# Kernel optimization log

Hardware: AMD Instinct MI355X
Metric: run time of the kernel (lower is better)

Reference implementation:

```python
import jax, jax.numpy as jnp
import numpy as np

D, P, R, K = 1024, 256, 64, 1024  # directions, sampling points, rank, subcarriers

def setup_inputs() -> dict:
    key = jax.random.key(0)
    k1, k2, k3 = jax.random.split(key, 3)
    return {
        "attenuation_vectors": jax.random.normal(k1, (D, P, R), dtype=jnp.float32),
        "radiation_vectors": jax.random.normal(k2, (D, P, R), dtype=jnp.float32),
        "frequency_basis_vectors": jax.random.normal(k3, (K, R), dtype=jnp.float32),
    }

def reference(attenuation_vectors, radiation_vectors, frequency_basis_vectors):
    # Original (per ray d, per subcarrier k):
    #   atten_factor[d,k] = sum_p sum_r u_rho[d,p,r] * F[k,r]
    #   rad_factor[d,k]   = sum_p sum_r u_s[d,p,r]   * F[k,r]
    #   csi[k] = (1/D) * sum_d atten_factor[d,k] * rad_factor[d,k]
    # Vectorized as two contractions over (p, r) plus a reduction over d.
    A = jnp.einsum('dpr,kr->dk', attenuation_vectors, frequency_basis_vectors)
    B = jnp.einsum('dpr,kr->dk', radiation_vectors, frequency_basis_vectors)
    num_directions = attenuation_vectors.shape[0]
    csi = jnp.sum(A * B, axis=0) / num_directions  # [K]
    return csi
```

## Files before the change

kernel.cpp:

```cpp
#include <hip/hip_runtime.h>

#define D_DIRS 1024
#define P_PTS  256
#define R_RANK 64
#define K_SUB  1024

typedef float v4f __attribute__((ext_vector_type(4)));

#define WS_A 0
#define WS_B (D_DIRS * R_RANK)
#define WS_M (2 * D_DIRS * R_RANK)
#define WS_MSUM 0
#define NB_B 32
#define DCHUNK (D_DIRS / NB_B)

__device__ __forceinline__ v4f ntload(const v4f* __restrict__ p) {
    return __builtin_nontemporal_load(p);
}

__device__ __forceinline__ v4f shfl_xor_v4(v4f v, int m) {
    v4f r;
    r.x = __shfl_xor(v.x, m);
    r.y = __shfl_xor(v.y, m);
    r.z = __shfl_xor(v.z, m);
    r.w = __shfl_xor(v.w, m);
    return r;
}

__global__ __launch_bounds__(512) void k_reduce_p(const float* __restrict__ atten,
                                                  const float* __restrict__ rad,
                                                  float* __restrict__ ws) {
    const int bid  = blockIdx.x;
    const int t    = threadIdx.x;
    const int lane = t & 63;
    const int wave = t >> 6;
    const int rq   = t & 15;

    const v4f* A4 = (const v4f*)atten;
    const v4f* B4 = (const v4f*)rad;

    __shared__ v4f lA[2][8][16];
    __shared__ v4f lB[2][8][16];

    const int d0 = bid * 4;

    v4f a_cur[8], b_cur[8], a_nxt[8], b_nxt[8];
    {
        const v4f* pa = A4 + (size_t)d0 * 4096 + t;
        const v4f* pb = B4 + (size_t)d0 * 4096 + t;
#pragma unroll
        for (int k = 0; k < 8; ++k) a_cur[k] = ntload(pa + k * 512);
#pragma unroll
        for (int k = 0; k < 8; ++k) b_cur[k] = ntload(pb + k * 512);
    }

#pragma unroll
    for (int dd = 0; dd < 4; ++dd) {
        const int d = d0 + dd;

        if (dd < 3) {
            const v4f* na = A4 + (size_t)(d + 1) * 4096 + t;
            const v4f* nb = B4 + (size_t)(d + 1) * 4096 + t;
#pragma unroll
            for (int k = 0; k < 8; ++k) a_nxt[k] = ntload(na + k * 512);
#pragma unroll
            for (int k = 0; k < 8; ++k) b_nxt[k] = ntload(nb + k * 512);
        }

        v4f sa = ((a_cur[0] + a_cur[1]) + (a_cur[2] + a_cur[3])) +
                 ((a_cur[4] + a_cur[5]) + (a_cur[6] + a_cur[7]));
        v4f sb = ((b_cur[0] + b_cur[1]) + (b_cur[2] + b_cur[3])) +
                 ((b_cur[4] + b_cur[5]) + (b_cur[6] + b_cur[7]));

        sa = sa + shfl_xor_v4(sa, 16);
        sa = sa + shfl_xor_v4(sa, 32);
        sb = sb + shfl_xor_v4(sb, 16);
        sb = sb + shfl_xor_v4(sb, 32);

        if ((lane >> 4) == 0) {
            lA[dd & 1][wave][rq] = sa;
            lB[dd & 1][wave][rq] = sb;
        }
        __syncthreads();

        if (t < 16) {
            v4f s = lA[dd & 1][0][t];
#pragma unroll
            for (int w = 1; w < 8; ++w) s = s + lA[dd & 1][w][t];
            ((v4f*)(ws + WS_A))[d * 16 + t] = s;
        } else if (t >= 64 && t < 80) {
            const int q = t - 64;
            v4f s = lB[dd & 1][0][q];
#pragma unroll
            for (int w = 1; w < 8; ++w) s = s + lB[dd & 1][w][q];
            ((v4f*)(ws + WS_B))[d * 16 + q] = s;
        }

#pragma unroll
        for (int k = 0; k < 8; ++k) { a_cur[k] = a_nxt[k]; b_cur[k] = b_nxt[k]; }
    }
}

__global__ __launch_bounds__(256) void k_partial_m(float* __restrict__ ws) {
    const int bb = blockIdx.x;
    const int t  = threadIdx.x;

    __shared__ float sa[DCHUNK * R_RANK];
    __shared__ float sb[DCHUNK * R_RANK];

    const float4* a4 = (const float4*)(ws + WS_A) + bb * (DCHUNK * R_RANK / 4);
    const float4* b4 = (const float4*)(ws + WS_B) + bb * (DCHUNK * R_RANK / 4);
    float4* sa4 = (float4*)sa;
    float4* sb4 = (float4*)sb;
    sa4[t]       = a4[t];
    sa4[t + 256] = a4[t + 256];
    sb4[t]       = b4[t];
    sb4[t + 256] = b4[t + 256];
    __syncthreads();

    const int c  = t & 63;
    const int wg = t >> 6;

    float acc[16];
#pragma unroll
    for (int i = 0; i < 16; ++i) acc[i] = 0.f;

    for (int dd = 0; dd < DCHUNK; ++dd) {
        const float bv = sb[dd * 64 + c];
        const float4* ar = (const float4*)&sa[dd * 64 + wg * 16];
        const float4 a0 = ar[0], a1 = ar[1], a2 = ar[2], a3 = ar[3];
        acc[0]  += a0.x * bv; acc[1]  += a0.y * bv; acc[2]  += a0.z * bv; acc[3]  += a0.w * bv;
        acc[4]  += a1.x * bv; acc[5]  += a1.y * bv; acc[6]  += a1.z * bv; acc[7]  += a1.w * bv;
        acc[8]  += a2.x * bv; acc[9]  += a2.y * bv; acc[10] += a2.z * bv; acc[11] += a2.w * bv;
        acc[12] += a3.x * bv; acc[13] += a3.y * bv; acc[14] += a3.z * bv; acc[15] += a3.w * bv;
    }

    float* Mp = ws + WS_M + bb * 4096;
#pragma unroll
    for (int i = 0; i < 16; ++i) Mp[(wg * 16 + i) * 64 + c] = acc[i];
}

__global__ __launch_bounds__(256) void k_reduce_m(float* __restrict__ ws) {
    const int tg = blockIdx.x * 256 + threadIdx.x;
    const float4* Mp4 = (const float4*)(ws + WS_M);
    float4 s = make_float4(0.f, 0.f, 0.f, 0.f);
#pragma unroll
    for (int g = 0; g < NB_B; ++g) {
        const float4 v = Mp4[g * 1024 + tg];
        s.x += v.x; s.y += v.y; s.z += v.z; s.w += v.w;
    }
    ((float4*)(ws + WS_MSUM))[tg] = s;
}

__global__ __launch_bounds__(256) void k_csi(const float* __restrict__ ws,
                                             const float* __restrict__ freq,
                                             float* __restrict__ out) {
    const int bb = blockIdx.x;
    const int t  = threadIdx.x;

    __shared__ float Ms[64 * 68];
    __shared__ float Fs[64 * 65];
    __shared__ float red[4][64];

    const float4* M4 = (const float4*)(ws + WS_MSUM);
#pragma unroll
    for (int i = 0; i < 4; ++i) {
        const int idx4 = i * 256 + t;
        const float4 s = M4[idx4];
        const int r = idx4 >> 4, c4 = idx4 & 15;
        *(float4*)&Ms[r * 68 + c4 * 4] = s;
    }

    const float4* F4 = (const float4*)freq + bb * 1024;
#pragma unroll
    for (int i = 0; i < 4; ++i) {
        const int idx4 = i * 256 + t;
        const float4 v = F4[idx4];
        const int row = idx4 >> 4, c4 = idx4 & 15;
        Fs[row * 65 + c4 * 4 + 0] = v.x;
        Fs[row * 65 + c4 * 4 + 1] = v.y;
        Fs[row * 65 + c4 * 4 + 2] = v.z;
        Fs[row * 65 + c4 * 4 + 3] = v.w;
    }
    __syncthreads();

    const int kl = t & 63;
    const int jg = t >> 6;

    float h[16];
#pragma unroll
    for (int j = 0; j < 16; ++j) h[j] = 0.f;

    for (int r = 0; r < 64; ++r) {
        const float fv = Fs[kl * 65 + r];
        const float4* mr = (const float4*)&Ms[r * 68 + jg * 16];
        const float4 m0 = mr[0], m1 = mr[1], m2 = mr[2], m3 = mr[3];
        h[0]  += fv * m0.x; h[1]  += fv * m0.y; h[2]  += fv * m0.z; h[3]  += fv * m0.w;
        h[4]  += fv * m1.x; h[5]  += fv * m1.y; h[6]  += fv * m1.z; h[7]  += fv * m1.w;
        h[8]  += fv * m2.x; h[9]  += fv * m2.y; h[10] += fv * m2.z; h[11] += fv * m2.w;
        h[12] += fv * m3.x; h[13] += fv * m3.y; h[14] += fv * m3.z; h[15] += fv * m3.w;
    }

    float part = 0.f;
#pragma unroll
    for (int j = 0; j < 16; ++j) part += h[j] * Fs[kl * 65 + jg * 16 + j];

    red[jg][kl] = part;
    __syncthreads();
    if (t < 64) {
        out[bb * 64 + t] =
            (red[0][t] + red[1][t] + red[2][t] + red[3][t]) * (1.0f / (float)D_DIRS);
    }
}

extern "C" void kernel_launch(void* const* d_in, const int* in_sizes, int n_in,
                              void* d_out, int out_size, void* d_ws, size_t ws_size,
                              hipStream_t stream) {
    const float* atten = (const float*)d_in[0];
    const float* rad   = (const float*)d_in[1];
    const float* freq  = (const float*)d_in[2];
    float* out = (float*)d_out;
    float* ws  = (float*)d_ws;

    k_reduce_p<<<D_DIRS / 4, 512, 0, stream>>>(atten, rad, ws);
    k_partial_m<<<NB_B, 256, 0, stream>>>(ws);
    k_reduce_m<<<4, 256, 0, stream>>>(ws);
    k_csi<<<16, 256, 0, stream>>>(ws, freq, out);
}
```

Before: 153.7 us.

## Remap P-reduction so each wave pair owns one direction, removing LDS and barriers

The sum over sampling points is reorganized so that each direction is handled by two waves, each owning half of the rank columns. Every lane accumulates 32 points across four prefetched chunks and finishes with in-wave xor shuffles, so the shared-memory staging and per-direction __syncthreads are gone. Each lane now reads 128-byte segments instead of fully contiguous 512-thread rows, which may change coalescing. The kernel is memory bound at 512MB, so the gain depends mostly on how well memory stays saturated.

```diff
diff --git a/kernel.cpp b/kernel.cpp
--- a/kernel.cpp
+++ b/kernel.cpp
@@ -30,74 +30,54 @@
 __global__ __launch_bounds__(512) void k_reduce_p(const float* __restrict__ atten,
                                                   const float* __restrict__ rad,
                                                   float* __restrict__ ws) {
-    const int bid  = blockIdx.x;
     const int t    = threadIdx.x;
+    const int wave = t >> 6;
     const int lane = t & 63;
-    const int wave = t >> 6;
-    const int rq   = t & 15;
-
-    const v4f* A4 = (const v4f*)atten;
-    const v4f* B4 = (const v4f*)rad;
-
-    __shared__ v4f lA[2][8][16];
-    __shared__ v4f lB[2][8][16];
-
-    const int d0 = bid * 4;
-
-    v4f a_cur[8], b_cur[8], a_nxt[8], b_nxt[8];
-    {
-        const v4f* pa = A4 + (size_t)d0 * 4096 + t;
-        const v4f* pb = B4 + (size_t)d0 * 4096 + t;
-#pragma unroll
-        for (int k = 0; k < 8; ++k) a_cur[k] = ntload(pa + k * 512);
-#pragma unroll
-        for (int k = 0; k < 8; ++k) b_cur[k] = ntload(pb + k * 512);
-    }
-
-#pragma unroll
-    for (int dd = 0; dd < 4; ++dd) {
-        const int d = d0 + dd;
-
-        if (dd < 3) {
-            const v4f* na = A4 + (size_t)(d + 1) * 4096 + t;
-            const v4f* nb = B4 + (size_t)(d + 1) * 4096 + t;
-#pragma unroll
-            for (int k = 0; k < 8; ++k) a_nxt[k] = ntload(na + k * 512);
-#pragma unroll
-            for (int k = 0; k < 8; ++k) b_nxt[k] = ntload(nb + k * 512);
+    const int d    = blockIdx.x * 4 + (wave >> 1);
+    const int half = wave & 1;
+    const int r4g  = lane & 7;
+    const int pr   = lane >> 3;
+
+    const int base = pr * 16 + half * 8 + r4g;
+    const v4f* A4 = (const v4f*)atten + (size_t)d * 4096 + base;
+    const v4f* B4 = (const v4f*)rad   + (size_t)d * 4096 + base;
+
+    v4f pa[8], pb[8], na[8], nb[8];
+#pragma unroll
+    for (int j = 0; j < 8; ++j) pa[j] = ntload(A4 + j * 128);
+#pragma unroll
+    for (int j = 0; j < 8; ++j) pb[j] = ntload(B4 + j * 128);
+
+    v4f acc_a = {0.f, 0.f, 0.f, 0.f};
+    v4f acc_b = {0.f, 0.f, 0.f, 0.f};
+
+#pragma unroll
+    for (int mc = 0; mc < 4; ++mc) {
+        if (mc < 3) {
+            const int off = (mc + 1) * 8 * 128;
+#pragma unroll
+            for (int j = 0; j < 8; ++j) na[j] = ntload(A4 + off + j * 128);
+#pragma unroll
+            for (int j = 0; j < 8; ++j) nb[j] = ntload(B4 + off + j * 128);
         }
-
-        v4f sa = ((a_cur[0] + a_cur[1]) + (a_cur[2] + a_cur[3])) +
-                 ((a_cur[4] + a_cur[5]) + (a_cur[6] + a_cur[7]));
-        v4f sb = ((b_cur[0] + b_cur[1]) + (b_cur[2] + b_cur[3])) +
-                 ((b_cur[4] + b_cur[5]) + (b_cur[6] + b_cur[7]));
-
-        sa = sa + shfl_xor_v4(sa, 16);
-        sa = sa + shfl_xor_v4(sa, 32);
-        sb = sb + shfl_xor_v4(sb, 16);
-        sb = sb + shfl_xor_v4(sb, 32);
-
-        if ((lane >> 4) == 0) {
-            lA[dd & 1][wave][rq] = sa;
-            lB[dd & 1][wave][rq] = sb;
-        }
-        __syncthreads();
-
-        if (t < 16) {
-            v4f s = lA[dd & 1][0][t];
-#pragma unroll
-            for (int w = 1; w < 8; ++w) s = s + lA[dd & 1][w][t];
-            ((v4f*)(ws + WS_A))[d * 16 + t] = s;
-        } else if (t >= 64 && t < 80) {
-            const int q = t - 64;
-            v4f s = lB[dd & 1][0][q];
-#pragma unroll
-            for (int w = 1; w < 8; ++w) s = s + lB[dd & 1][w][q];
-            ((v4f*)(ws + WS_B))[d * 16 + q] = s;
-        }
-
-#pragma unroll
-        for (int k = 0; k < 8; ++k) { a_cur[k] = a_nxt[k]; b_cur[k] = b_nxt[k]; }
+        acc_a = acc_a + (((pa[0] + pa[1]) + (pa[2] + pa[3])) +
+                         ((pa[4] + pa[5]) + (pa[6] + pa[7])));
+        acc_b = acc_b + (((pb[0] + pb[1]) + (pb[2] + pb[3])) +
+                         ((pb[4] + pb[5]) + (pb[6] + pb[7])));
+#pragma unroll
+        for (int j = 0; j < 8; ++j) { pa[j] = na[j]; pb[j] = nb[j]; }
+    }
+
+    acc_a = acc_a + shfl_xor_v4(acc_a, 8);
+    acc_a = acc_a + shfl_xor_v4(acc_a, 16);
+    acc_a = acc_a + shfl_xor_v4(acc_a, 32);
+    acc_b = acc_b + shfl_xor_v4(acc_b, 8);
+    acc_b = acc_b + shfl_xor_v4(acc_b, 16);
+    acc_b = acc_b + shfl_xor_v4(acc_b, 32);
+
+    if (pr == 0) {
+        ((v4f*)(ws + WS_A))[d * 16 + half * 8 + r4g] = acc_a;
+        ((v4f*)(ws + WS_B))[d * 16 + half * 8 + r4g] = acc_b;
     }
 }
 
```

Result: faster. 149.4 us (-2.8%).
